# Performance work log

Hardware: AMD Instinct MI355X
Metric: run time of the kernel (lower is better)

The kernel has to match this reference:

```python
import jax, jax.numpy as jnp
import numpy as np

GRID = 14  # encoded_image_size

def _grid_edge_index():
    # Exact replica of build_adjacency_matrix().nonzero(): 8-neighbor 14x14 grid.
    edges = []
    for r in range(GRID):
        for c in range(GRID):
            i = r * GRID + c
            for rr in range(max(0, r - 1), min(r + 2, GRID)):
                for cc in range(max(0, c - 1), min(c + 2, GRID)):
                    if rr == r and cc == c:
                        continue
                    edges.append((i, rr * GRID + cc))
    return np.asarray(edges, dtype=np.int64).T  # (2, 1404)


def setup_inputs() -> dict:
    key = jax.random.key(0)
    k1, k2, k3 = jax.random.split(key, 3)
    B, H, W, C, Hid = 128, 14, 14, 2048, 1024
    x = jax.random.normal(k1, (B, H, W, C), dtype=jnp.float32)
    edge_index = jnp.asarray(_grid_edge_index())
    W1 = jax.random.normal(k2, (C, Hid), dtype=jnp.float32) * (1.0 / np.sqrt(C))
    b1 = jnp.zeros((Hid,), jnp.float32)
    W2 = jax.random.normal(k3, (Hid, C), dtype=jnp.float32) * (1.0 / np.sqrt(Hid))
    b2 = jnp.zeros((C,), jnp.float32)
    return {"x": x, "edge_index": edge_index, "W1": W1, "b1": b1, "W2": W2, "b2": b2}


def _gcn_conv(h, W, b, src, dst, dinv):
    # PyG GCNConv: linear transform, symmetric deg-normalized (A+I) aggregation, bias.
    h = h @ W  # [N, out]
    norm = (dinv[src] * dinv[dst])[:, None]
    agg = jax.ops.segment_sum(h[src] * norm, dst, num_segments=h.shape[0])
    agg = agg + h * (dinv * dinv)[:, None]  # self-loop term, norm = 1/deg_i
    return agg + b


def reference(x, edge_index, W1, b1, W2, b2):
    B, H, Wd, C = x.shape
    N = B * H * Wd
    # Faithful to original: permute(0,3,1,2) then reshape(-1, C) (layout-scrambling).
    xf = jnp.transpose(x, (0, 3, 1, 2)).reshape(-1, C)  # [N, C]
    src, dst = edge_index[0], edge_index[1]
    # Degrees over ALL N nodes: self-loop (=1) everywhere + incoming grid edges
    # (only first 196 nodes have grid neighbors; rest are passthrough).
    deg = jnp.ones((N,), xf.dtype).at[dst].add(1.0)
    dinv = jax.lax.rsqrt(deg)
    h = jax.nn.relu(_gcn_conv(xf, W1, b1, src, dst, dinv))
    h = jax.nn.relu(_gcn_conv(h, W2, b2, src, dst, dinv))
    # reshape + permute(0,3,1,2) + permute(0,2,3,1) == identity back to NHWC.
    return h.reshape(B, H, Wd, C)
```

## Files before the change

kernel.cpp:

```cpp
#include <hip/hip_runtime.h>

typedef float  float4_t __attribute__((ext_vector_type(4)));
typedef __bf16 bf16x8   __attribute__((ext_vector_type(8)));

#define BM 128
#define BN 128
#define BK 64

#define GLD16(g, l)                                                        \
    __builtin_amdgcn_global_load_lds(                                      \
        (const __attribute__((address_space(1))) void*)(g),                \
        (__attribute__((address_space(3))) void*)(l), 16, 0, 0)

__global__ __launch_bounds__(256)
void transpose_x_kernel(const float* __restrict__ x, __bf16* __restrict__ A1)
{
    __shared__ float sm[32 * 221];
    const int b  = blockIdx.y;
    const int c0 = blockIdx.x * 32;
    const int t  = threadIdx.x;

    const float* xb = x + (size_t)b * 401408;
    const int cl = t & 31;
    const int p0 = t >> 5;
#pragma unroll
    for (int k = 0; k < 25; ++k) {
        int p = p0 + k * 8;
        if (p < 196)
            sm[cl * 221 + p + (p >> 3)] = xb[(size_t)p * 2048 + c0 + cl];
    }
    __syncthreads();

    __bf16* ab = A1 + (size_t)b * 401408 + (size_t)c0 * 196;
#pragma unroll
    for (int k = 0; k < 4; ++k) {
        int o8 = k * 256 + t;
        if (o8 < 784) {
            int o  = o8 * 8;
            int cc = o / 196;
            int pp = o - cc * 196;
            bf16x8 v;
#pragma unroll
            for (int i = 0; i < 8; ++i) {
                v[i] = (__bf16)sm[cc * 221 + pp + (pp >> 3)];
                if (++pp == 196) { pp = 0; ++cc; }
            }
            *(bf16x8*)(ab + o) = v;
        }
    }
}

__global__ void transpose_w_kernel(const float* __restrict__ W, __bf16* __restrict__ Wt,
                                   int K, int N)
{
    __shared__ float tile[32][33];
    const int kt = blockIdx.x * 32, nt = blockIdx.y * 32;
    const int tx = threadIdx.x, ty = threadIdx.y;
#pragma unroll
    for (int rr = 0; rr < 4; ++rr)
        tile[ty + rr * 8][tx] = W[(size_t)(kt + ty + rr * 8) * N + nt + tx];
    __syncthreads();
#pragma unroll
    for (int rr = 0; rr < 4; ++rr)
        Wt[(size_t)(nt + ty + rr * 8) * K + kt + tx] = (__bf16)tile[tx][ty + rr * 8];
}

template<bool OUT_BF16, int NX, int G>
__global__ __launch_bounds__(256)
void gemm_bt_kernel(const __bf16* __restrict__ A,
                    const __bf16* __restrict__ Bt,
                    const float* __restrict__ bias,
                    void* __restrict__ out,
                    float* __restrict__ raw_out,
                    int M, int N, int K)
{
    __shared__ __bf16 sA[BM * BK];
    __shared__ __bf16 sB[BN * BK];

    const int tid  = threadIdx.x;
    const int wid  = tid >> 6;
    const int lane = tid & 63;

    constexpr int NGROUPS = NX / G;
    constexpr int XPG     = 8 / NGROUPS;
    const int l   = blockIdx.x + NX * blockIdx.y;
    const int r8  = l & 7;
    const int t   = l >> 3;
    const int gid = r8 % NGROUPS;
    const int s   = r8 / NGROUPS;
    const int row0 = ((t / G) * XPG + s) * BM;
    const int col0 = (gid * G + (t % G)) * BN;

    const int wave_m = (wid >> 1) * 64;
    const int wave_n = (wid & 1) * 64;

    float4_t acc[4][4];
#pragma unroll
    for (int i = 0; i < 4; ++i)
#pragma unroll
        for (int j = 0; j < 4; ++j)
            acc[i][j] = (float4_t){0.f, 0.f, 0.f, 0.f};

    const int lrow = lane >> 3;
    const int lcol = ((lane & 7) ^ lrow) * 8;
    const int mrow = lane & 15;
    const int kq   = (lane >> 4) * 8;

    for (int k0 = 0; k0 < K; k0 += BK) {
        const __bf16* Ab = A  + (size_t)row0 * K + k0;
        const __bf16* Bb = Bt + (size_t)col0 * K + k0;
#pragma unroll
        for (int tt = 0; tt < 4; ++tt) {
            int chunk = wid * 4 + tt;
            int rr = chunk * 8 + lrow;
            GLD16(Ab + (size_t)rr * K + lcol, sA + chunk * 512);
            GLD16(Bb + (size_t)rr * K + lcol, sB + chunk * 512);
        }
        __syncthreads();
#pragma unroll
        for (int kk = 0; kk < BK; kk += 32) {
            bf16x8 af[4], bfr[4];
            const int g0 = (kk + kq) >> 3;
#pragma unroll
            for (int i = 0; i < 4; ++i) {
                int row = wave_m + i * 16 + mrow;
                af[i] = *(const bf16x8*)&sA[row * BK + ((g0 ^ (row & 7)) << 3)];
            }
#pragma unroll
            for (int j = 0; j < 4; ++j) {
                int row = wave_n + j * 16 + mrow;
                bfr[j] = *(const bf16x8*)&sB[row * BK + ((g0 ^ (row & 7)) << 3)];
            }
#pragma unroll
            for (int i = 0; i < 4; ++i)
#pragma unroll
                for (int j = 0; j < 4; ++j)
                    acc[i][j] = __builtin_amdgcn_mfma_f32_16x16x32_bf16(
                        af[i], bfr[j], acc[i][j], 0, 0, 0);
        }
        __syncthreads();
    }

    const int crow = (lane >> 4) * 4;
    const int ccol = lane & 15;
    const bool has_raw = row0 < 196;
#pragma unroll
    for (int i = 0; i < 4; ++i) {
#pragma unroll
        for (int j = 0; j < 4; ++j) {
            int gcol = col0 + wave_n + j * 16 + ccol;
            float bv = bias[gcol];
#pragma unroll
            for (int r = 0; r < 4; ++r) {
                int grow = row0 + wave_m + i * 16 + crow + r;
                float v = acc[i][j][r];
                if (has_raw && grow < 196) raw_out[grow * N + gcol] = v;
                float o = fmaxf(v + bv, 0.f);
                if (OUT_BF16) ((__bf16*)out)[(size_t)grow * N + gcol] = (__bf16)o;
                else          ((float*)out)[(size_t)grow * N + gcol] = o;
            }
        }
    }
}

template<typename OutT>
__global__ void fixup_kernel(const float* __restrict__ raw, const float* __restrict__ bias,
                             OutT* __restrict__ out, int N)
{
    const int q = blockIdx.x;
    const int r = q / 14, c = q % 14;
    int nbr[8];
    int cnt = 0;
    for (int rr = (r > 0 ? r - 1 : 0); rr <= (r < 13 ? r + 1 : 13); ++rr)
        for (int cc = (c > 0 ? c - 1 : 0); cc <= (c < 13 ? c + 1 : 13); ++cc)
            if (!(rr == r && cc == c)) nbr[cnt++] = rr * 14 + cc;
    const float dq    = 1.f / sqrtf(1.f + (float)cnt);
    const float wself = 1.f / (1.f + (float)cnt);
    float wn[8];
    for (int t = 0; t < cnt; ++t) {
        int pr = nbr[t] / 14, pc = nbr[t] % 14;
        int pcnt = ((pr < 13 ? pr + 1 : 13) - (pr > 0 ? pr - 1 : 0) + 1) *
                   ((pc < 13 ? pc + 1 : 13) - (pc > 0 ? pc - 1 : 0) + 1) - 1;
        wn[t] = dq / sqrtf(1.f + (float)pcnt);
    }
    const int ch = blockIdx.y * 256 + threadIdx.x;
    float s = raw[q * N + ch] * wself;
    for (int t = 0; t < cnt; ++t) s += raw[nbr[t] * N + ch] * wn[t];
    float o = fmaxf(s + bias[ch], 0.f);
    out[(size_t)q * N + ch] = (OutT)o;
}

extern "C" void kernel_launch(void* const* d_in, const int* in_sizes, int n_in,
                              void* d_out, int out_size, void* d_ws, size_t ws_size,
                              hipStream_t stream)
{
    const float* x  = (const float*)d_in[0];
    const float* W1 = (const float*)d_in[2];
    const float* b1 = (const float*)d_in[3];
    const float* W2 = (const float*)d_in[4];
    const float* b2 = (const float*)d_in[5];

    const int M = 25088, C = 2048, Hid = 1024;

    __bf16* A1 = (__bf16*)d_out;

    char* ws = (char*)d_ws;
    __bf16* A2    = (__bf16*)(ws);
    __bf16* W1t   = (__bf16*)(ws + 51380224);
    __bf16* W2t   = (__bf16*)(ws + 55574528);
    float*  h1raw = (float*)(ws + 59768832);
    float*  h2raw = (float*)(ws + 60571648);

    transpose_x_kernel<<<dim3(64, 128), 256, 0, stream>>>(x, A1);
    transpose_w_kernel<<<dim3(C / 32, Hid / 32), dim3(32, 8), 0, stream>>>(W1, W1t, C, Hid);
    transpose_w_kernel<<<dim3(Hid / 32, C / 32), dim3(32, 8), 0, stream>>>(W2, W2t, Hid, C);

    gemm_bt_kernel<true, 8, 2><<<dim3(Hid / BN, M / BM), 256, 0, stream>>>(
        A1, W1t, b1, (void*)A2, h1raw, M, Hid, C);
    fixup_kernel<__bf16><<<dim3(196, Hid / 256), 256, 0, stream>>>(h1raw, b1, A2, Hid);

    gemm_bt_kernel<false, 16, 4><<<dim3(C / BN, M / BM), 256, 0, stream>>>(
        A2, W2t, b2, d_out, h2raw, M, C, Hid);
    fixup_kernel<float><<<dim3(196, C / 256), 256, 0, stream>>>(h2raw, b2, (float*)d_out, C);
}
```

Measured before the change: 684.5 us.

## Triple-buffer GEMM LDS tiles with 256-row blocks and interleaved prefetch

The GEMM now uses 256x128 tiles with 512 threads (8 waves) and a three-stage LDS ring. Global-to-LDS loads for tile t+2 are split into two halves and issued between MFMA phases, using explicit waitcnt, barriers and setprio in place of a full sync per K step. The block-to-tile mapping is simplified into XCD-aware column grouping, and the x transpose now reads float4 vectors. The aim is to hide load latency and raise MFMA utilisation. In exchange it uses more LDS and registers per block and relies on hand-tuned wait counts being correct.

```diff
diff --git a/kernel.cpp b/kernel.cpp
--- a/kernel.cpp
+++ b/kernel.cpp
@@ -3,7 +3,7 @@
 typedef float  float4_t __attribute__((ext_vector_type(4)));
 typedef __bf16 bf16x8   __attribute__((ext_vector_type(8)));
 
-#define BM 128
+#define BM 256
 #define BN 128
 #define BK 64
 
@@ -21,13 +21,17 @@
     const int t  = threadIdx.x;
 
     const float* xb = x + (size_t)b * 401408;
-    const int cl = t & 31;
-    const int p0 = t >> 5;
-#pragma unroll
-    for (int k = 0; k < 25; ++k) {
-        int p = p0 + k * 8;
-        if (p < 196)
-            sm[cl * 221 + p + (p >> 3)] = xb[(size_t)p * 2048 + c0 + cl];
+    const int c4 = (t & 7) * 4;
+    const int p0 = t >> 3;
+#pragma unroll
+    for (int k = 0; k < 7; ++k) {
+        int p = p0 + k * 32;
+        if (p < 196) {
+            float4_t v = *(const float4_t*)&xb[(size_t)p * 2048 + c0 + c4];
+#pragma unroll
+            for (int i = 0; i < 4; ++i)
+                sm[(c4 + i) * 221 + p + (p >> 3)] = v[i];
+        }
     }
     __syncthreads();
 
@@ -65,8 +69,8 @@
         Wt[(size_t)(nt + ty + rr * 8) * K + kt + tx] = (__bf16)tile[tx][ty + rr * 8];
 }
 
-template<bool OUT_BF16, int NX, int G>
-__global__ __launch_bounds__(256)
+template<bool OUT_BF16>
+__global__ __launch_bounds__(512, 2)
 void gemm_bt_kernel(const __bf16* __restrict__ A,
                     const __bf16* __restrict__ Bt,
                     const float* __restrict__ bias,
@@ -74,22 +78,21 @@
                     float* __restrict__ raw_out,
                     int M, int N, int K)
 {
-    __shared__ __bf16 sA[BM * BK];
-    __shared__ __bf16 sB[BN * BK];
+    __shared__ __bf16 lds[3 * 24576];
 
     const int tid  = threadIdx.x;
     const int wid  = tid >> 6;
     const int lane = tid & 63;
 
-    constexpr int NGROUPS = NX / G;
-    constexpr int XPG     = 8 / NGROUPS;
-    const int l   = blockIdx.x + NX * blockIdx.y;
-    const int r8  = l & 7;
-    const int t   = l >> 3;
-    const int gid = r8 % NGROUPS;
-    const int s   = r8 / NGROUPS;
-    const int row0 = ((t / G) * XPG + s) * BM;
-    const int col0 = (gid * G + (t % G)) * BN;
+    const int nx  = gridDim.x, ny = gridDim.y;
+    const int lid = blockIdx.x + nx * blockIdx.y;
+    const int xcd = lid & 7;
+    const int i0  = lid >> 3;
+    const int gn  = nx >> 3;
+    const int nl  = i0 / ny;
+    const int mi  = i0 - nl * ny;
+    const int row0 = mi * BM;
+    const int col0 = (xcd * gn + nl) * BN;
 
     const int wave_m = (wid >> 1) * 64;
     const int wave_n = (wid & 1) * 64;
@@ -101,49 +104,108 @@
         for (int j = 0; j < 4; ++j)
             acc[i][j] = (float4_t){0.f, 0.f, 0.f, 0.f};
 
-    const int lrow = lane >> 3;
-    const int lcol = ((lane & 7) ^ lrow) * 8;
-    const int mrow = lane & 15;
-    const int kq   = (lane >> 4) * 8;
-
-    for (int k0 = 0; k0 < K; k0 += BK) {
-        const __bf16* Ab = A  + (size_t)row0 * K + k0;
-        const __bf16* Bb = Bt + (size_t)col0 * K + k0;
-#pragma unroll
-        for (int tt = 0; tt < 4; ++tt) {
-            int chunk = wid * 4 + tt;
-            int rr = chunk * 8 + lrow;
-            GLD16(Ab + (size_t)rr * K + lcol, sA + chunk * 512);
-            GLD16(Bb + (size_t)rr * K + lcol, sB + chunk * 512);
-        }
-        __syncthreads();
-#pragma unroll
-        for (int kk = 0; kk < BK; kk += 32) {
-            bf16x8 af[4], bfr[4];
-            const int g0 = (kk + kq) >> 3;
-#pragma unroll
-            for (int i = 0; i < 4; ++i) {
-                int row = wave_m + i * 16 + mrow;
-                af[i] = *(const bf16x8*)&sA[row * BK + ((g0 ^ (row & 7)) << 3)];
-            }
-#pragma unroll
-            for (int j = 0; j < 4; ++j) {
-                int row = wave_n + j * 16 + mrow;
-                bfr[j] = *(const bf16x8*)&sB[row * BK + ((g0 ^ (row & 7)) << 3)];
-            }
-#pragma unroll
-            for (int i = 0; i < 4; ++i)
+    const int    srow  = (wid << 3) + (lane >> 3);
+    const int    scol  = ((lane & 7) ^ (lane >> 3)) << 3;
+    const int    wb    = wid << 9;
+    const __bf16* gA   = A  + (size_t)(row0 + srow) * K + scol;
+    const __bf16* gB   = Bt + (size_t)(col0 + srow) * K + scol;
+    const size_t rstep = (size_t)64 * K;
+
+#define STAGE_P1(t, da) do {                                   \
+    const __bf16* ga = gA + (size_t)(t) * BK;                  \
+    GLD16(ga,             (da) +         wb);                  \
+    GLD16(ga +     rstep, (da) + 4096  + wb);                  \
+    GLD16(ga + 2 * rstep, (da) + 8192  + wb);                  \
+} while (0)
+#define STAGE_P2(t, da) do {                                   \
+    const __bf16* ga = gA + (size_t)(t) * BK + 3 * rstep;      \
+    const __bf16* gb = gB + (size_t)(t) * BK;                  \
+    GLD16(ga,             (da) + 12288 + wb);                  \
+    GLD16(gb,             (da) + 16384 + wb);                  \
+    GLD16(gb +     rstep, (da) + 20480 + wb);                  \
+} while (0)
+
+    STAGE_P1(0, lds);         STAGE_P2(0, lds);
+    STAGE_P1(1, lds + 24576); STAGE_P2(1, lds + 24576);
+    asm volatile("s_waitcnt vmcnt(6)" ::: "memory");
+    __builtin_amdgcn_s_barrier();
+    __builtin_amdgcn_sched_barrier(0);
+
+    const int xorv = lane & 7;
+    const int kq   = lane >> 4;
+    const int swz0 = (kq ^ xorv) << 3;
+    const int arow = (wave_m + (lane & 15)) * 64;
+    const int brow = (wave_n + (lane & 15)) * 64;
+
+    const int NTt = K / BK;
+    int cur = 0, st2 = 2;
+    for (int t = 0; t < NTt; ++t) {
+        const __bf16* cA = lds + cur * 24576;
+        const __bf16* cB = cA + 16384;
+        __bf16* dst2 = lds + st2 * 24576;
+        const bool do_stage = (t < NTt - 2);
+
+        bf16x8 bfr[2][4], af0[2][2];
+#pragma unroll
+        for (int x = 0; x < 2; ++x) {
+            const int sz = swz0 ^ (x << 5);
+#pragma unroll
+            for (int j = 0; j < 4; ++j)
+                bfr[x][j] = *(const bf16x8*)&cB[brow + j * 1024 + sz];
+#pragma unroll
+            for (int i = 0; i < 2; ++i)
+                af0[x][i] = *(const bf16x8*)&cA[arow + i * 1024 + sz];
+        }
+        if (do_stage) STAGE_P1(t + 2, dst2);
+        __builtin_amdgcn_s_barrier();
+        __builtin_amdgcn_sched_barrier(0);
+        __builtin_amdgcn_s_setprio(1);
+#pragma unroll
+        for (int x = 0; x < 2; ++x)
+#pragma unroll
+            for (int i = 0; i < 2; ++i)
 #pragma unroll
                 for (int j = 0; j < 4; ++j)
                     acc[i][j] = __builtin_amdgcn_mfma_f32_16x16x32_bf16(
-                        af[i], bfr[j], acc[i][j], 0, 0, 0);
-        }
-        __syncthreads();
-    }
+                        af0[x][i], bfr[x][j], acc[i][j], 0, 0, 0);
+        __builtin_amdgcn_s_setprio(0);
+
+        bf16x8 af1[2][2];
+#pragma unroll
+        for (int x = 0; x < 2; ++x) {
+            const int sz = swz0 ^ (x << 5);
+#pragma unroll
+            for (int i = 0; i < 2; ++i)
+                af1[x][i] = *(const bf16x8*)&cA[arow + (i + 2) * 1024 + sz];
+        }
+        if (do_stage) STAGE_P2(t + 2, dst2);
+        if (t < NTt - 1) {
+            asm volatile("s_waitcnt lgkmcnt(0)" ::: "memory");
+            if (do_stage) asm volatile("s_waitcnt vmcnt(6)" ::: "memory");
+            else          asm volatile("s_waitcnt vmcnt(0)" ::: "memory");
+            __builtin_amdgcn_s_barrier();
+            __builtin_amdgcn_sched_barrier(0);
+        }
+        __builtin_amdgcn_s_setprio(1);
+#pragma unroll
+        for (int x = 0; x < 2; ++x)
+#pragma unroll
+            for (int i = 0; i < 2; ++i)
+#pragma unroll
+                for (int j = 0; j < 4; ++j)
+                    acc[i + 2][j] = __builtin_amdgcn_mfma_f32_16x16x32_bf16(
+                        af1[x][i], bfr[x][j], acc[i + 2][j], 0, 0, 0);
+        __builtin_amdgcn_s_setprio(0);
+
+        cur = (cur == 2) ? 0 : cur + 1;
+        st2 = (st2 == 2) ? 0 : st2 + 1;
+    }
+#undef STAGE_P1
+#undef STAGE_P2
 
     const int crow = (lane >> 4) * 4;
     const int ccol = lane & 15;
-    const bool has_raw = row0 < 196;
+    const bool has_raw = (row0 == 0);
 #pragma unroll
     for (int i = 0; i < 4; ++i) {
 #pragma unroll
@@ -215,11 +277,11 @@
     transpose_w_kernel<<<dim3(C / 32, Hid / 32), dim3(32, 8), 0, stream>>>(W1, W1t, C, Hid);
     transpose_w_kernel<<<dim3(Hid / 32, C / 32), dim3(32, 8), 0, stream>>>(W2, W2t, Hid, C);
 
-    gemm_bt_kernel<true, 8, 2><<<dim3(Hid / BN, M / BM), 256, 0, stream>>>(
+    gemm_bt_kernel<true><<<dim3(Hid / BN, M / BM), 512, 0, stream>>>(
         A1, W1t, b1, (void*)A2, h1raw, M, Hid, C);
     fixup_kernel<__bf16><<<dim3(196, Hid / 256), 256, 0, stream>>>(h1raw, b1, A2, Hid);
 
-    gemm_bt_kernel<false, 16, 4><<<dim3(C / BN, M / BM), 256, 0, stream>>>(
+    gemm_bt_kernel<false><<<dim3(C / BN, M / BM), 512, 0, stream>>>(
         A2, W2t, b2, d_out, h2raw, M, C, Hid);
     fixup_kernel<float><<<dim3(196, C / 256), 256, 0, stream>>>(h2raw, b2, (float*)d_out, C);
 }
```

New measurement: 681.3 us. About the same (-0.5%).
